# Kernel optimization log

Hardware: AMD Instinct MI355X
Metric: run time of the kernel (lower is better)

The kernel has to match this reference:

```python
import jax, jax.numpy as jnp
import numpy as np

N, E, NREL = 50000, 800000, 4
IN, EMB, HID, OUT, LVL = 32, 32, 32, 32, 3


def setup_inputs() -> dict:
    key = jax.random.key(0)
    ks = jax.random.split(key, 24)
    f32 = jnp.float32
    inp = {
        'x': jax.random.normal(ks[0], (N, IN), f32),
        'node_feat': jax.random.normal(ks[1], (N, EMB), f32),
        'edge_feat': jax.random.normal(ks[2], (E, EMB), f32),
        'src': jax.random.randint(ks[3], (E,), 0, N, jnp.int32),
        'dst': jax.random.randint(ks[4], (E,), 0, N, jnp.int32),
        'eid': jax.random.randint(ks[5], (E,), 0, NREL, jnp.int32),
        # layer 1 (in_feat=IN)
        'Wr1': jax.random.normal(ks[6], (NREL, IN + 2 * EMB, HID), f32) * 0.1,
        'attn_w1': jax.random.normal(ks[7], (EMB + HID, 1), f32) * 0.1,
        'loop_w1': jax.random.normal(ks[8], (EMB, HID), f32) * 0.1,
        'h_bias1': jax.random.normal(ks[9], (HID,), f32) * 0.1,
        'amrm_W1': jax.random.normal(ks[10], (LVL, HID, HID), f32) * 0.1,
        'amrm_b1': jax.random.normal(ks[11], (LVL, HID), f32) * 0.1,
        'amrm_a1': jax.random.normal(ks[12], (HID, 1), f32) * 0.1,
        # layer 2 (in_feat=HID)
        'Wr2': jax.random.normal(ks[13], (NREL, HID + 2 * EMB, OUT), f32) * 0.1,
        'attn_w2': jax.random.normal(ks[14], (EMB + OUT, 1), f32) * 0.1,
        'loop_w2': jax.random.normal(ks[15], (EMB, OUT), f32) * 0.1,
        'h_bias2': jax.random.normal(ks[16], (OUT,), f32) * 0.1,
        'amrm_W2': jax.random.normal(ks[17], (LVL, OUT, OUT), f32) * 0.1,
        'amrm_b2': jax.random.normal(ks[18], (LVL, OUT), f32) * 0.1,
        'amrm_a2': jax.random.normal(ks[19], (OUT, 1), f32) * 0.1,
    }
    return inp


def _rp_layer(feat, node_feat, src, dst, eid, edge_feat,
              Wr, attn_w, loop_w, h_bias, amrm_W, amrm_b, amrm_a):
    n = node_feat.shape[0]
    ones_e = jnp.ones((src.shape[0],), feat.dtype)
    # symmetric-ish degree norm: feat scaled by out-degree^-1/2
    deg_out = jnp.clip(jax.ops.segment_sum(ones_e, src, num_segments=n), 1.0)
    feat = feat * (deg_out ** -0.5)[:, None]
    # per-edge gather + relation-typed linear (grouped GEMM over NREL types)
    xe = jnp.concatenate([feat[src], edge_feat, node_feat[dst]], axis=1)  # [E, in+2*emb]
    m = jnp.zeros((xe.shape[0], Wr.shape[2]), feat.dtype)
    for r in range(Wr.shape[0]):
        m = m + jnp.where((eid == r)[:, None], xe @ Wr[r], 0.0)
    # edge attention + segment softmax over incoming edges per dst node
    z = jax.nn.leaky_relu(jnp.concatenate([node_feat[dst], m], axis=1) @ attn_w)  # [E,1]
    zmax = jax.ops.segment_max(z, dst, num_segments=n)
    ez = jnp.exp(z - zmax[dst])
    a = ez / jax.ops.segment_sum(ez, dst, num_segments=n)[dst]
    # scatter-sum aggregation
    h = jax.ops.segment_sum(a * m, dst, num_segments=n)
    h = h + node_feat @ loop_w
    deg_in = jnp.clip(jax.ops.segment_sum(ones_e, dst, num_segments=n), 1.0)
    h = h * (deg_in ** -0.5)[:, None] + h_bias
    # adaptive multi-level relation module
    lv = jax.nn.relu(jnp.einsum('nh,lho->nlo', h, amrm_W) + amrm_b[None])  # [N,L,O]
    sc = jax.nn.softmax(jnp.einsum('nlo,o->nl', lv, amrm_a[:, 0]), axis=-1)  # [N,L]
    return jnp.einsum('nl,nlo->no', sc, lv)


def reference(x, node_feat, edge_feat, src, dst, eid,
              Wr1, attn_w1, loop_w1, h_bias1, amrm_W1, amrm_b1, amrm_a1,
              Wr2, attn_w2, loop_w2, h_bias2, amrm_W2, amrm_b2, amrm_a2):
    h = jax.nn.relu(_rp_layer(x, node_feat, src, dst, eid, edge_feat,
                              Wr1, attn_w1, loop_w1, h_bias1, amrm_W1, amrm_b1, amrm_a1))
    h = jax.nn.relu(_rp_layer(h, node_feat, src, dst, eid, edge_feat,
                              Wr2, attn_w2, loop_w2, h_bias2, amrm_W2, amrm_b2, amrm_a2))
    return h
```

## Files before the change

### kernel.cpp

```cpp
#include <hip/hip_runtime.h>

#define NN 50000
#define NE 800000

#define O_DEGIN   0
#define O_DEGOUT  50048
#define O_ROWPTR  100096
#define O_CURSOR  150208
#define O_EINFO   200256
#define O_FEATN   1800256
#define O_ZF      3400256
#define O_ZNRD    3600320
#define O_VV      3800384
#define O_EZ      3800832
#define O_NFT     4600832
#define O_WDENT   6200832
#define O_YACCT   6450880
#define O_H1      19250880
#define O_PACC    20850880


__global__ __launch_bounds__(256) void k_deg(const int* __restrict__ src,
                                             const int* __restrict__ dst,
                                             int* degin, int* degout) {
    int e = blockIdx.x * 256 + threadIdx.x;
    if (e < NE) {
        atomicAdd(&degin[dst[e]], 1);
        atomicAdd(&degout[src[e]], 1);
    }
}

__global__ __launch_bounds__(1024) void k_scan(const int* __restrict__ degin,
                                               int* rowptr, int* cursor) {
    __shared__ int swsum[16];
    __shared__ int stot;
    int t = threadIdx.x;
    int lane = t & 63, w = t >> 6;
    int carry = 0;
    for (int ch = 0; ch < 4; ch++) {
        int base = ch * 16384 + t * 16;
        int v[16];
        int s = 0;
#pragma unroll
        for (int j = 0; j < 16; j++) {
            v[j] = (base + j < NN) ? degin[base + j] : 0;
            s += v[j];
        }
        int incl = s;
#pragma unroll
        for (int off = 1; off < 64; off <<= 1) {
            int x = __shfl_up(incl, off, 64);
            if (lane >= off) incl += x;
        }
        if (lane == 63) swsum[w] = incl;
        __syncthreads();
        if (w == 0) {
            int y = (lane < 16) ? swsum[lane] : 0;
            int yi = y;
#pragma unroll
            for (int off = 1; off < 16; off <<= 1) {
                int x = __shfl_up(yi, off, 64);
                if (lane >= off) yi += x;
            }
            if (lane < 16) swsum[lane] = yi - y;
            if (lane == 15) stot = yi;
        }
        __syncthreads();
        int excl = carry + swsum[w] + (incl - s);
#pragma unroll
        for (int j = 0; j < 16; j++) {
            if (base + j < NN) { rowptr[base + j] = excl; cursor[base + j] = excl; }
            excl += v[j];
        }
        carry += stot;
        __syncthreads();
    }
    if (t == 0) rowptr[NN] = carry;
}

__global__ __launch_bounds__(256) void k_scatter(const int* __restrict__ src,
                                                 const int* __restrict__ dst,
                                                 const int* __restrict__ eid,
                                                 int* cursor, int2* einfo) {
    int e = blockIdx.x * 256 + threadIdx.x;
    if (e >= NE) return;
    int slot = atomicAdd(&cursor[dst[e]], 1);
    einfo[slot] = make_int2(src[e] | (eid[e] << 20), e);
}


__global__ __launch_bounds__(384) void k_prevec(const float* __restrict__ Wr,
                                                const float* __restrict__ attw,
                                                float* __restrict__ vvec) {
    int t = threadIdx.x;
    int r = (t >> 5) & 3, k = t & 31, part = t >> 7;
    int row = (part == 0) ? (32 + k) : (part == 1) ? k : (64 + k);
    const float* wrow = Wr + (size_t)r * 3072 + row * 32;
    float s = 0.f;
#pragma unroll
    for (int c = 0; c < 32; c++) s += wrow[c] * attw[32 + c];
    vvec[t] = s;
}

__global__ __launch_bounds__(128) void k_nodeproj(const float* __restrict__ feat,
                                                  const float* __restrict__ nfeat,
                                                  const float* __restrict__ attw,
                                                  const float* __restrict__ vvec,
                                                  const int* __restrict__ degout,
                                                  float* __restrict__ featn,
                                                  float* __restrict__ nfT,
                                                  float* __restrict__ zF,
                                                  float* __restrict__ znrd) {
    int n = blockIdx.x * 128 + threadIdx.x;
    if (n >= NN) return;
    int dg = degout[n];
    float sc0 = rsqrtf((float)(dg > 1 ? dg : 1));
    const float* fin = feat + (size_t)n * 32;
    const float* nin = nfeat + (size_t)n * 32;
    float fv[32], nv[32];
#pragma unroll
    for (int k = 0; k < 32; k += 4) {
        float4 f4 = *(const float4*)&fin[k];
        fv[k] = f4.x * sc0; fv[k + 1] = f4.y * sc0;
        fv[k + 2] = f4.z * sc0; fv[k + 3] = f4.w * sc0;
        float4 n4 = *(const float4*)&nin[k];
        nv[k] = n4.x; nv[k + 1] = n4.y; nv[k + 2] = n4.z; nv[k + 3] = n4.w;
    }
    float* fo = featn + (size_t)n * 32;
#pragma unroll
    for (int k = 0; k < 32; k += 4)
        *(float4*)&fo[k] = make_float4(fv[k], fv[k + 1], fv[k + 2], fv[k + 3]);
#pragma unroll
    for (int k = 0; k < 32; k++) nfT[(size_t)k * NN + n] = nv[k];
    float zn = 0.f;
#pragma unroll
    for (int k = 0; k < 32; k++) zn += nv[k] * attw[k];
#pragma unroll
    for (int r = 0; r < 4; r++) {
        float zf = 0.f, zd = 0.f;
        const float* vf = vvec + 128 + r * 32;
        const float* vd = vvec + 256 + r * 32;
#pragma unroll
        for (int k = 0; k < 32; k++) { zf += fv[k] * vf[k]; zd += nv[k] * vd[k]; }
        zF[r * NN + n] = zf;
        znrd[r * NN + n] = zn + zd;
    }
}

__global__ __launch_bounds__(256) void k_ez(const int* __restrict__ src,
                                            const int* __restrict__ dst,
                                            const int* __restrict__ eid,
                                            const float* __restrict__ efeat,
                                            const float* __restrict__ zF,
                                            const float* __restrict__ znrd,
                                            const float* __restrict__ vvec,
                                            float* __restrict__ ez) {
    int e = blockIdx.x * 256 + threadIdx.x;
    int s = src[e], d = dst[e], r = eid[e];
    const float* er = efeat + (size_t)e * 32;
    float d0 = 0.f, d1 = 0.f, d2 = 0.f, d3 = 0.f;
#pragma unroll
    for (int k = 0; k < 32; k += 4) {
        float4 f = *(const float4*)&er[k];
        d0 += f.x * vvec[k]       + f.y * vvec[k + 1]
            + f.z * vvec[k + 2]   + f.w * vvec[k + 3];
        d1 += f.x * vvec[32 + k]  + f.y * vvec[33 + k]
            + f.z * vvec[34 + k]  + f.w * vvec[35 + k];
        d2 += f.x * vvec[64 + k]  + f.y * vvec[65 + k]
            + f.z * vvec[66 + k]  + f.w * vvec[67 + k];
        d3 += f.x * vvec[96 + k]  + f.y * vvec[97 + k]
            + f.z * vvec[98 + k]  + f.w * vvec[99 + k];
    }
    float dot = (r == 0) ? d0 : (r == 1) ? d1 : (r == 2) ? d2 : d3;
    float z = znrd[r * NN + d] + zF[r * NN + s] + dot;
    z = z > 0.f ? z : 0.01f * z;
    ez[e] = __expf(z);
}

__global__ __launch_bounds__(512) void k_agg(const int* __restrict__ rowptr,
                                             const int2* __restrict__ einfo,
                                             const float* __restrict__ ez,
                                             const float* __restrict__ efeat,
                                             const float* __restrict__ featn,
                                             float* __restrict__ yaccT,
                                             float* __restrict__ wdenT) {
    __shared__ float sT[256 * 9];
    int tid = threadIdx.x;
    int lane = tid & 63;
    int wid = tid >> 6;
    int n0 = blockIdx.x * 8;
    int n = n0 + wid;
    int c = lane & 31;
    int p = lane >> 5;

    int rp0 = rowptr[n];
    int deg = rowptr[n + 1] - rp0;

    float yf0 = 0.f, yf1 = 0.f, yf2 = 0.f, yf3 = 0.f;
    float ye0 = 0.f, ye1 = 0.f, ye2 = 0.f, ye3 = 0.f;
    float w0 = 0.f, w1 = 0.f, w2 = 0.f, w3 = 0.f, den = 0.f;

    int2 meA = make_int2(0, 0), meB = make_int2(0, 0);
    float ezA = 0.f, efA = 0.f, fnA = 0.f;
    if (p < deg) {
        meA = einfo[rp0 + p];
        ezA = ez[meA.y];
        efA = efeat[(size_t)meA.y * 32 + c];
        fnA = featn[(size_t)(meA.x & 0xFFFFF) * 32 + c];
    }
    if (p + 2 < deg) meB = einfo[rp0 + p + 2];

    for (int t = p; t < deg; t += 2) {
        float ezB = 0.f, efB = 0.f, fnB = 0.f;
        int2 meC = make_int2(0, 0);
        if (t + 2 < deg) {
            ezB = ez[meB.y];
            efB = efeat[(size_t)meB.y * 32 + c];
            fnB = featn[(size_t)(meB.x & 0xFFFFF) * 32 + c];
        }
        if (t + 4 < deg) meC = einfo[rp0 + t + 4];
        int rb = meA.x >> 20;
        float e0 = (rb == 0) ? ezA : 0.f;
        float e1 = (rb == 1) ? ezA : 0.f;
        float e2 = (rb == 2) ? ezA : 0.f;
        float e3 = (rb == 3) ? ezA : 0.f;
        yf0 += e0 * fnA; yf1 += e1 * fnA; yf2 += e2 * fnA; yf3 += e3 * fnA;
        ye0 += e0 * efA; ye1 += e1 * efA; ye2 += e2 * efA; ye3 += e3 * efA;
        w0 += e0; w1 += e1; w2 += e2; w3 += e3;
        den += ezA;
        meA = meB; ezA = ezB; efA = efB; fnA = fnB; meB = meC;
    }

    yf0 += __shfl_xor(yf0, 32); yf1 += __shfl_xor(yf1, 32);
    yf2 += __shfl_xor(yf2, 32); yf3 += __shfl_xor(yf3, 32);
    ye0 += __shfl_xor(ye0, 32); ye1 += __shfl_xor(ye1, 32);
    ye2 += __shfl_xor(ye2, 32); ye3 += __shfl_xor(ye3, 32);
    w0 += __shfl_xor(w0, 32); w1 += __shfl_xor(w1, 32);
    w2 += __shfl_xor(w2, 32); w3 += __shfl_xor(w3, 32);
    den += __shfl_xor(den, 32);

    if (lane < 5) {
        float wv = (lane == 0) ? w0 : (lane == 1) ? w1 : (lane == 2) ? w2
                 : (lane == 3) ? w3 : den;
        wdenT[lane * NN + n] = wv;
    }

    {
        int kb = 128 * p + c;
        sT[(kb +  0) * 9 + wid] = p ? ye0 : yf0;
        sT[(kb + 32) * 9 + wid] = p ? ye1 : yf1;
        sT[(kb + 64) * 9 + wid] = p ? ye2 : yf2;
        sT[(kb + 96) * 9 + wid] = p ? ye3 : yf3;
    }
    __syncthreads();
    int k = tid >> 1, hf = tid & 1;
    float4 v = make_float4(sT[k * 9 + hf * 4 + 0], sT[k * 9 + hf * 4 + 1],
                           sT[k * 9 + hf * 4 + 2], sT[k * 9 + hf * 4 + 3]);
    *(float4*)&yaccT[(size_t)k * NN + n0 + hf * 4] = v;
}

__global__ __launch_bounds__(256) void k_postA(const float* __restrict__ yaccT,
                                               const float* __restrict__ wdenT,
                                               const float* __restrict__ nfT,
                                               const float* __restrict__ Wr,
                                               float* __restrict__ pacc) {
    int n = blockIdx.x * 256 + threadIdx.x;
    if (n >= NN) return;
    int r = blockIdx.y;

    float nv[32];
#pragma unroll
    for (int k = 0; k < 32; k++) nv[k] = nfT[(size_t)k * NN + n];
    float wr = wdenT[r * NN + n];

    const float* W = Wr + (size_t)r * 3072;
    const float* ufc = yaccT + (size_t)(r * 32) * NN + n;
    const float* uec = yaccT + (size_t)(128 + r * 32) * NN + n;

    float acc[32];
#pragma unroll
    for (int i = 0; i < 32; i++) acc[i] = 0.f;
    for (int k4 = 0; k4 < 32; k4 += 4) {
        float a0 = ufc[(size_t)(k4 + 0) * NN], a1 = ufc[(size_t)(k4 + 1) * NN];
        float a2 = ufc[(size_t)(k4 + 2) * NN], a3 = ufc[(size_t)(k4 + 3) * NN];
        float b0 = uec[(size_t)(k4 + 0) * NN], b1 = uec[(size_t)(k4 + 1) * NN];
        float b2 = uec[(size_t)(k4 + 2) * NN], b3 = uec[(size_t)(k4 + 3) * NN];
        float g0 = wr * nv[k4],     g1 = wr * nv[k4 + 1];
        float g2 = wr * nv[k4 + 2], g3 = wr * nv[k4 + 3];
        const float* Wk = W + k4 * 32;
#pragma unroll
        for (int i = 0; i < 32; i++)
            acc[i] += a0 * Wk[i]        + a1 * Wk[32 + i]
                    + a2 * Wk[64 + i]   + a3 * Wk[96 + i]
                    + b0 * Wk[1024 + i] + b1 * Wk[1056 + i]
                    + b2 * Wk[1088 + i] + b3 * Wk[1120 + i]
                    + g0 * Wk[2048 + i] + g1 * Wk[2080 + i]
                    + g2 * Wk[2112 + i] + g3 * Wk[2144 + i];
    }
    float* po = pacc + (size_t)(r * 32) * NN + n;
#pragma unroll
    for (int i = 0; i < 32; i++) po[(size_t)i * NN] = acc[i];
}

__global__ __launch_bounds__(256) void k_postB(const int* __restrict__ rowptr,
                                               const float* __restrict__ pacc,
                                               const float* __restrict__ wdenT,
                                               const float* __restrict__ nfT,
                                               const float* __restrict__ lw,
                                               const float* __restrict__ hbias,
                                               const float* __restrict__ aW,
                                               const float* __restrict__ ab,
                                               const float* __restrict__ aa,
                                               float* __restrict__ out) {
    int n = blockIdx.x * 256 + threadIdx.x;
    if (n >= NN) return;
    int deg = rowptr[n + 1] - rowptr[n];
    float den = wdenT[4 * NN + n];
    float invden = (deg > 0) ? 1.f / den : 0.f;

    float nv[32];
#pragma unroll
    for (int k = 0; k < 32; k++) nv[k] = nfT[(size_t)k * NN + n];

    float h[32];
#pragma unroll
    for (int i = 0; i < 32; i++) {
        float s = pacc[(size_t)i * NN + n]
                + pacc[(size_t)(32 + i) * NN + n]
                + pacc[(size_t)(64 + i) * NN + n]
                + pacc[(size_t)(96 + i) * NN + n];
        h[i] = s * invden;
    }
    for (int k4 = 0; k4 < 32; k4 += 4) {
        const float* Lk = lw + k4 * 32;
#pragma unroll
        for (int i = 0; i < 32; i++)
            h[i] += nv[k4] * Lk[i] + nv[k4 + 1] * Lk[32 + i]
                  + nv[k4 + 2] * Lk[64 + i] + nv[k4 + 3] * Lk[96 + i];
    }
    float hsc = rsqrtf((float)(deg > 1 ? deg : 1));
#pragma unroll
    for (int i = 0; i < 32; i++) h[i] = h[i] * hsc + hbias[i];

    float acc[32];
    float s[3];
#pragma unroll
    for (int l = 0; l < 3; l++) {
        const float* A = aW + (size_t)l * 1024;
#pragma unroll
        for (int i = 0; i < 32; i++) acc[i] = ab[l * 32 + i];
        for (int k4 = 0; k4 < 32; k4 += 4) {
            const float* Ak = A + k4 * 32;
#pragma unroll
            for (int i = 0; i < 32; i++)
                acc[i] += h[k4] * Ak[i] + h[k4 + 1] * Ak[32 + i]
                        + h[k4 + 2] * Ak[64 + i] + h[k4 + 3] * Ak[96 + i];
        }
        float sl = 0.f;
#pragma unroll
        for (int i = 0; i < 32; i++) {
            float lv = acc[i] > 0.f ? acc[i] : 0.f;
            sl += lv * aa[i];
        }
        s[l] = sl;
    }
    float mx = fmaxf(s[0], fmaxf(s[1], s[2]));
    float e0 = __expf(s[0] - mx), e1 = __expf(s[1] - mx), e2 = __expf(s[2] - mx);
    float inv = 1.f / (e0 + e1 + e2);
    float scl[3] = {e0 * inv, e1 * inv, e2 * inv};

    float outv[32];
#pragma unroll
    for (int i = 0; i < 32; i++) outv[i] = 0.f;
#pragma unroll
    for (int l = 0; l < 3; l++) {
        const float* A = aW + (size_t)l * 1024;
#pragma unroll
        for (int i = 0; i < 32; i++) acc[i] = ab[l * 32 + i];
        for (int k4 = 0; k4 < 32; k4 += 4) {
            const float* Ak = A + k4 * 32;
#pragma unroll
            for (int i = 0; i < 32; i++)
                acc[i] += h[k4] * Ak[i] + h[k4 + 1] * Ak[32 + i]
                        + h[k4 + 2] * Ak[64 + i] + h[k4 + 3] * Ak[96 + i];
        }
#pragma unroll
        for (int i = 0; i < 32; i++) {
            float lv = acc[i] > 0.f ? acc[i] : 0.f;
            outv[i] += scl[l] * lv;
        }
    }
    float* op = out + (size_t)n * 32;
#pragma unroll
    for (int i = 0; i < 32; i += 4)
        *(float4*)&op[i] = make_float4(fmaxf(outv[i], 0.f), fmaxf(outv[i + 1], 0.f),
                                       fmaxf(outv[i + 2], 0.f), fmaxf(outv[i + 3], 0.f));
}


static void launch_layer(const float* feat, const float* nf, const float* efeat,
                         const int* src, const int* dst, const int* eid,
                         const float* Wr, const float* attw, const float* lw,
                         const float* hb, const float* aW, const float* ab,
                         const float* aa, float* wsf, int* wsi, float* out,
                         hipStream_t stream) {
    k_prevec<<<1, 384, 0, stream>>>(Wr, attw, wsf + O_VV);
    k_nodeproj<<<391, 128, 0, stream>>>(feat, nf, attw, wsf + O_VV, wsi + O_DEGOUT,
                                        wsf + O_FEATN, wsf + O_NFT,
                                        wsf + O_ZF, wsf + O_ZNRD);
    k_ez<<<3125, 256, 0, stream>>>(src, dst, eid, efeat, wsf + O_ZF, wsf + O_ZNRD,
                                   wsf + O_VV, wsf + O_EZ);
    k_agg<<<6250, 512, 0, stream>>>(wsi + O_ROWPTR, (const int2*)(wsi + O_EINFO),
                                    wsf + O_EZ, efeat, wsf + O_FEATN,
                                    wsf + O_YACCT, wsf + O_WDENT);
    k_postA<<<dim3(196, 4), 256, 0, stream>>>(wsf + O_YACCT, wsf + O_WDENT,
                                              wsf + O_NFT, Wr, wsf + O_PACC);
    k_postB<<<196, 256, 0, stream>>>(wsi + O_ROWPTR, wsf + O_PACC, wsf + O_WDENT,
                                     wsf + O_NFT, lw, hb, aW, ab, aa, out);
}

extern "C" void kernel_launch(void* const* d_in, const int* in_sizes, int n_in,
                              void* d_out, int out_size, void* d_ws, size_t ws_size,
                              hipStream_t stream) {
    const float* x     = (const float*)d_in[0];
    const float* nfeat = (const float*)d_in[1];
    const float* efeat = (const float*)d_in[2];
    const int*   src   = (const int*)d_in[3];
    const int*   dst   = (const int*)d_in[4];
    const int*   eid   = (const int*)d_in[5];
    const float* Wr1   = (const float*)d_in[6];
    const float* attw1 = (const float*)d_in[7];
    const float* lw1   = (const float*)d_in[8];
    const float* hb1   = (const float*)d_in[9];
    const float* aW1   = (const float*)d_in[10];
    const float* ab1   = (const float*)d_in[11];
    const float* aa1   = (const float*)d_in[12];
    const float* Wr2   = (const float*)d_in[13];
    const float* attw2 = (const float*)d_in[14];
    const float* lw2   = (const float*)d_in[15];
    const float* hb2   = (const float*)d_in[16];
    const float* aW2   = (const float*)d_in[17];
    const float* ab2   = (const float*)d_in[18];
    const float* aa2   = (const float*)d_in[19];

    float* wsf = (float*)d_ws;
    int*   wsi = (int*)d_ws;
    float* out = (float*)d_out;

    hipMemsetAsync(d_ws, 0, (size_t)O_ROWPTR * 4, stream);

    k_deg<<<NE / 256, 256, 0, stream>>>(src, dst, wsi + O_DEGIN, wsi + O_DEGOUT);
    k_scan<<<1, 1024, 0, stream>>>(wsi + O_DEGIN, wsi + O_ROWPTR, wsi + O_CURSOR);
    k_scatter<<<NE / 256, 256, 0, stream>>>(src, dst, eid, wsi + O_CURSOR,
                                            (int2*)(wsi + O_EINFO));

    launch_layer(x, nfeat, efeat, src, dst, eid, Wr1, attw1, lw1, hb1, aW1, ab1, aa1,
                 wsf, wsi, wsf + O_H1, stream);
    launch_layer(wsf + O_H1, nfeat, efeat, src, dst, eid, Wr2, attw2, lw2, hb2,
                 aW2, ab2, aa2, wsf, wsi, out, stream);
}
```

Baseline: 703.8 us.

## Merge prevec launches, index relation vector directly, unroll agg loop by two

The two per-layer prevec launches become a single two-block launch that writes both layers' attention vectors, which removes one kernel launch. The workspace offsets are shifted to fit the larger vector buffer. The edge-score kernel now computes only the dot product for the edge's own relation, reading its vector with float4 loads, instead of computing all four and selecting one. The aggregation loop drops the software-pipelined prefetch in favour of processing two edges per iteration with independent loads, and one GEMM loop in the post-processing kernel is fully unrolled, which may raise register pressure.

```diff
diff --git a/kernel.cpp b/kernel.cpp
--- a/kernel.cpp
+++ b/kernel.cpp
@@ -12,12 +12,12 @@
 #define O_ZF      3400256
 #define O_ZNRD    3600320
 #define O_VV      3800384
-#define O_EZ      3800832
-#define O_NFT     4600832
-#define O_WDENT   6200832
-#define O_YACCT   6450880
-#define O_H1      19250880
-#define O_PACC    20850880
+#define O_EZ      3801216
+#define O_NFT     4601216
+#define O_WDENT   6201216
+#define O_YACCT   6451328
+#define O_H1      19251328
+#define O_PACC    20851328
 
 
 __global__ __launch_bounds__(256) void k_deg(const int* __restrict__ src,
@@ -89,9 +89,14 @@
 }
 
 
-__global__ __launch_bounds__(384) void k_prevec(const float* __restrict__ Wr,
-                                                const float* __restrict__ attw,
+__global__ __launch_bounds__(384) void k_prevec(const float* __restrict__ Wr1,
+                                                const float* __restrict__ attw1,
+                                                const float* __restrict__ Wr2,
+                                                const float* __restrict__ attw2,
                                                 float* __restrict__ vvec) {
+    const float* Wr = blockIdx.x ? Wr2 : Wr1;
+    const float* attw = blockIdx.x ? attw2 : attw1;
+    float* vv = vvec + blockIdx.x * 384;
     int t = threadIdx.x;
     int r = (t >> 5) & 3, k = t & 31, part = t >> 7;
     int row = (part == 0) ? (32 + k) : (part == 1) ? k : (64 + k);
@@ -99,7 +104,7 @@
     float s = 0.f;
 #pragma unroll
     for (int c = 0; c < 32; c++) s += wrow[c] * attw[32 + c];
-    vvec[t] = s;
+    vv[t] = s;
 }
 
 __global__ __launch_bounds__(128) void k_nodeproj(const float* __restrict__ feat,
@@ -158,20 +163,14 @@
     int e = blockIdx.x * 256 + threadIdx.x;
     int s = src[e], d = dst[e], r = eid[e];
     const float* er = efeat + (size_t)e * 32;
-    float d0 = 0.f, d1 = 0.f, d2 = 0.f, d3 = 0.f;
+    const float* vr = vvec + r * 32;
+    float dot = 0.f;
 #pragma unroll
     for (int k = 0; k < 32; k += 4) {
         float4 f = *(const float4*)&er[k];
-        d0 += f.x * vvec[k]       + f.y * vvec[k + 1]
-            + f.z * vvec[k + 2]   + f.w * vvec[k + 3];
-        d1 += f.x * vvec[32 + k]  + f.y * vvec[33 + k]
-            + f.z * vvec[34 + k]  + f.w * vvec[35 + k];
-        d2 += f.x * vvec[64 + k]  + f.y * vvec[65 + k]
-            + f.z * vvec[66 + k]  + f.w * vvec[67 + k];
-        d3 += f.x * vvec[96 + k]  + f.y * vvec[97 + k]
-            + f.z * vvec[98 + k]  + f.w * vvec[99 + k];
-    }
-    float dot = (r == 0) ? d0 : (r == 1) ? d1 : (r == 2) ? d2 : d3;
+        float4 v = *(const float4*)&vr[k];
+        dot += f.x * v.x + f.y * v.y + f.z * v.z + f.w * v.w;
+    }
     float z = znrd[r * NN + d] + zF[r * NN + s] + dot;
     z = z > 0.f ? z : 0.01f * z;
     ez[e] = __expf(z);
@@ -200,35 +199,47 @@
     float ye0 = 0.f, ye1 = 0.f, ye2 = 0.f, ye3 = 0.f;
     float w0 = 0.f, w1 = 0.f, w2 = 0.f, w3 = 0.f, den = 0.f;
 
-    int2 meA = make_int2(0, 0), meB = make_int2(0, 0);
-    float ezA = 0.f, efA = 0.f, fnA = 0.f;
-    if (p < deg) {
-        meA = einfo[rp0 + p];
-        ezA = ez[meA.y];
-        efA = efeat[(size_t)meA.y * 32 + c];
-        fnA = featn[(size_t)(meA.x & 0xFFFFF) * 32 + c];
-    }
-    if (p + 2 < deg) meB = einfo[rp0 + p + 2];
-
-    for (int t = p; t < deg; t += 2) {
-        float ezB = 0.f, efB = 0.f, fnB = 0.f;
-        int2 meC = make_int2(0, 0);
-        if (t + 2 < deg) {
-            ezB = ez[meB.y];
-            efB = efeat[(size_t)meB.y * 32 + c];
-            fnB = featn[(size_t)(meB.x & 0xFFFFF) * 32 + c];
-        }
-        if (t + 4 < deg) meC = einfo[rp0 + t + 4];
-        int rb = meA.x >> 20;
-        float e0 = (rb == 0) ? ezA : 0.f;
-        float e1 = (rb == 1) ? ezA : 0.f;
-        float e2 = (rb == 2) ? ezA : 0.f;
-        float e3 = (rb == 3) ? ezA : 0.f;
-        yf0 += e0 * fnA; yf1 += e1 * fnA; yf2 += e2 * fnA; yf3 += e3 * fnA;
-        ye0 += e0 * efA; ye1 += e1 * efA; ye2 += e2 * efA; ye3 += e3 * efA;
+    int t = p;
+    for (; t + 2 < deg; t += 4) {
+        int2 meA = einfo[rp0 + t];
+        int2 meB = einfo[rp0 + t + 2];
+        float ezA = ez[meA.y];
+        float ezB = ez[meB.y];
+        float efA = efeat[(size_t)meA.y * 32 + c];
+        float efB = efeat[(size_t)meB.y * 32 + c];
+        float fnA = featn[(size_t)(meA.x & 0xFFFFF) * 32 + c];
+        float fnB = featn[(size_t)(meB.x & 0xFFFFF) * 32 + c];
+        int rA = meA.x >> 20;
+        int rB = meB.x >> 20;
+        float a0 = (rA == 0) ? ezA : 0.f;
+        float a1 = (rA == 1) ? ezA : 0.f;
+        float a2 = (rA == 2) ? ezA : 0.f;
+        float a3 = (rA == 3) ? ezA : 0.f;
+        float b0 = (rB == 0) ? ezB : 0.f;
+        float b1 = (rB == 1) ? ezB : 0.f;
+        float b2 = (rB == 2) ? ezB : 0.f;
+        float b3 = (rB == 3) ? ezB : 0.f;
+        yf0 += a0 * fnA; yf1 += a1 * fnA; yf2 += a2 * fnA; yf3 += a3 * fnA;
+        ye0 += a0 * efA; ye1 += a1 * efA; ye2 += a2 * efA; ye3 += a3 * efA;
+        yf0 += b0 * fnB; yf1 += b1 * fnB; yf2 += b2 * fnB; yf3 += b3 * fnB;
+        ye0 += b0 * efB; ye1 += b1 * efB; ye2 += b2 * efB; ye3 += b3 * efB;
+        w0 += a0 + b0; w1 += a1 + b1; w2 += a2 + b2; w3 += a3 + b3;
+        den += ezA + ezB;
+    }
+    if (t < deg) {
+        int2 me = einfo[rp0 + t];
+        float ezv = ez[me.y];
+        float ef = efeat[(size_t)me.y * 32 + c];
+        float fn = featn[(size_t)(me.x & 0xFFFFF) * 32 + c];
+        int rb = me.x >> 20;
+        float e0 = (rb == 0) ? ezv : 0.f;
+        float e1 = (rb == 1) ? ezv : 0.f;
+        float e2 = (rb == 2) ? ezv : 0.f;
+        float e3 = (rb == 3) ? ezv : 0.f;
+        yf0 += e0 * fn; yf1 += e1 * fn; yf2 += e2 * fn; yf3 += e3 * fn;
+        ye0 += e0 * ef; ye1 += e1 * ef; ye2 += e2 * ef; ye3 += e3 * ef;
         w0 += e0; w1 += e1; w2 += e2; w3 += e3;
-        den += ezA;
-        meA = meB; ezA = ezB; efA = efB; fnA = fnB; meB = meC;
+        den += ezv;
     }
 
     yf0 += __shfl_xor(yf0, 32); yf1 += __shfl_xor(yf1, 32);
@@ -280,6 +291,7 @@
     float acc[32];
 #pragma unroll
     for (int i = 0; i < 32; i++) acc[i] = 0.f;
+#pragma unroll
     for (int k4 = 0; k4 < 32; k4 += 4) {
         float a0 = ufc[(size_t)(k4 + 0) * NN], a1 = ufc[(size_t)(k4 + 1) * NN];
         float a2 = ufc[(size_t)(k4 + 2) * NN], a3 = ufc[(size_t)(k4 + 3) * NN];
@@ -402,14 +414,13 @@
                          const int* src, const int* dst, const int* eid,
                          const float* Wr, const float* attw, const float* lw,
                          const float* hb, const float* aW, const float* ab,
-                         const float* aa, float* wsf, int* wsi, float* out,
-                         hipStream_t stream) {
-    k_prevec<<<1, 384, 0, stream>>>(Wr, attw, wsf + O_VV);
-    k_nodeproj<<<391, 128, 0, stream>>>(feat, nf, attw, wsf + O_VV, wsi + O_DEGOUT,
+                         const float* aa, const float* vv,
+                         float* wsf, int* wsi, float* out, hipStream_t stream) {
+    k_nodeproj<<<391, 128, 0, stream>>>(feat, nf, attw, vv, wsi + O_DEGOUT,
                                         wsf + O_FEATN, wsf + O_NFT,
                                         wsf + O_ZF, wsf + O_ZNRD);
     k_ez<<<3125, 256, 0, stream>>>(src, dst, eid, efeat, wsf + O_ZF, wsf + O_ZNRD,
-                                   wsf + O_VV, wsf + O_EZ);
+                                   vv, wsf + O_EZ);
     k_agg<<<6250, 512, 0, stream>>>(wsi + O_ROWPTR, (const int2*)(wsi + O_EINFO),
                                     wsf + O_EZ, efeat, wsf + O_FEATN,
                                     wsf + O_YACCT, wsf + O_WDENT);
@@ -453,9 +464,10 @@
     k_scan<<<1, 1024, 0, stream>>>(wsi + O_DEGIN, wsi + O_ROWPTR, wsi + O_CURSOR);
     k_scatter<<<NE / 256, 256, 0, stream>>>(src, dst, eid, wsi + O_CURSOR,
                                             (int2*)(wsi + O_EINFO));
+    k_prevec<<<2, 384, 0, stream>>>(Wr1, attw1, Wr2, attw2, wsf + O_VV);
 
     launch_layer(x, nfeat, efeat, src, dst, eid, Wr1, attw1, lw1, hb1, aW1, ab1, aa1,
-                 wsf, wsi, wsf + O_H1, stream);
+                 wsf + O_VV, wsf, wsi, wsf + O_H1, stream);
     launch_layer(wsf + O_H1, nfeat, efeat, src, dst, eid, Wr2, attw2, lw2, hb2,
-                 aW2, ab2, aa2, wsf, wsi, out, stream);
-}
+                 aW2, ab2, aa2, wsf + O_VV + 384, wsf, wsi, out, stream);
+}
```

Result: slower. 719.9 us (+2.3%).
